# Optimization experiments

Measured on AMD Instinct MI355X. Metric: run time of the kernel, lower is better.

The kernel has to match this reference:

```python
import jax, jax.numpy as jnp
import numpy as np

N, DIM, TOPK = 8192, 512, 10


def setup_inputs() -> dict:
    key = jax.random.key(0)
    k1, k2, k3, k4, k5 = jax.random.split(key, 5)
    s = DIM ** -0.5
    return {
        "X": jax.random.normal(k1, (N, DIM), dtype=jnp.float32),
        "Wh": jax.random.normal(k2, (DIM, DIM), dtype=jnp.float32) * s,
        "bh": jax.random.normal(k3, (DIM,), dtype=jnp.float32) * s,
        "Wt": jax.random.normal(k4, (DIM, DIM), dtype=jnp.float32) * s,
        "bt": jax.random.normal(k5, (DIM,), dtype=jnp.float32) * s,
    }


def reference(X, Wh, bh, Wt, bt):
    n, dim = X.shape
    scale = dim ** -0.5
    e_h = X @ Wh.T + bh                      # [n, dim]
    e_t = X @ Wt.T + bt                      # [n, dim]
    logits = (e_h @ e_t.T) * scale           # [n, n]
    topk_val, topk_idx = jax.lax.top_k(logits, TOPK)   # [n, k]
    weights = jax.nn.softmax(topk_val, axis=-1)        # [n, k]
    src = jnp.repeat(jnp.arange(n, dtype=jnp.int32), TOPK)  # [n*k]
    dst = topk_idx.reshape(-1).astype(jnp.int32)
    edge_index = jnp.stack([src, dst], axis=0)          # [2, n*k]
    edge_weight = weights.reshape(-1)                   # [n*k]
    return edge_index, edge_weight
```

## Files before the change

kernel.cpp:

```cpp
#include <hip/hip_runtime.h>
#include <math.h>

#define NROWS 8192
#define DIMK  512
#define TOPK  10
#define SCALE 0.044194173824159223f

#define ETM 128
#define ETN 128
#define ETK 16
#define NTHREADS 256

#define BM 128
#define BN 256
#define BK 32
#define NS2 16
#define SCOLS2 (NROWS / NS2)
#define NQ 256
#define CAP 64
#define TMARGIN 2.0f

typedef __attribute__((ext_vector_type(8))) short bf16x8;
typedef __attribute__((ext_vector_type(4))) float f32x4;
typedef __attribute__((ext_vector_type(2))) float f32x2;

__device__ __forceinline__ unsigned short f2bf(float f) {
  unsigned int u = __float_as_uint(f);
  u = (u + 0x7FFF + ((u >> 16) & 1)) >> 16;
  return (unsigned short)u;
}

__device__ __forceinline__ void gld16(const void* g, const void* lds) {
  __builtin_amdgcn_global_load_lds(
      (const __attribute__((address_space(1))) void*)g,
      (__attribute__((address_space(3))) void*)lds, 16, 0, 0);
}

__device__ __forceinline__ f32x2 pk_fma(f32x2 a, f32x2 b, f32x2 c) {
#if __has_builtin(__builtin_elementwise_fma)
  return __builtin_elementwise_fma(a, b, c);
#else
  f32x2 r; r[0] = fmaf(a[0], b[0], c[0]); r[1] = fmaf(a[1], b[1], c[1]);
  return r;
#endif
}

__global__ __launch_bounds__(NTHREADS, 2)
void embed_gemm(const float* __restrict__ X,
                const float* __restrict__ Wh, const float* __restrict__ bh,
                const float* __restrict__ Wt, const float* __restrict__ bt,
                float* __restrict__ Eh, float* __restrict__ Et,
                unsigned short* __restrict__ Ehb, unsigned short* __restrict__ Etb) {
  __shared__ float As[2][ETK][ETM + 4];
  __shared__ float Bs[2][ETK][ETN + 4];

  const int tid = threadIdx.x;
  const int rowBase = blockIdx.x * ETM;
  const int colBase = blockIdx.y * ETN;
  const float* W  = (colBase < DIMK) ? Wh : Wt;
  const float* bb = (colBase < DIMK) ? bh : bt;
  float* Out            = (colBase < DIMK) ? Eh : Et;
  unsigned short* Outb  = (colBase < DIMK) ? Ehb : Etb;
  const int colOff = colBase & (DIMK - 1);

  const int tx = tid & 15, ty = tid >> 4;
  f32x2 acc2[8][4];
#pragma unroll
  for (int r = 0; r < 8; ++r)
#pragma unroll
    for (int p = 0; p < 4; ++p) acc2[r][p] = (f32x2){0.f, 0.f};

  auto stage = [&](int buf, int kt) {
#pragma unroll
    for (int u = 0; u < 2; ++u) {
      const int idx = tid + u * NTHREADS;
      const int r = idx >> 2;
      const int dc = idx & 3;
      const float4 av = *(const float4*)&X[(size_t)(rowBase + r) * DIMK + kt + dc * 4];
      As[buf][dc * 4 + 0][r] = av.x; As[buf][dc * 4 + 1][r] = av.y;
      As[buf][dc * 4 + 2][r] = av.z; As[buf][dc * 4 + 3][r] = av.w;
    }
#pragma unroll
    for (int u = 0; u < 2; ++u) {
      const int idx = tid + u * NTHREADS;
      const int r = idx >> 2;
      const int dc = idx & 3;
      const float4 bv = *(const float4*)&W[(size_t)(colOff + r) * DIMK + kt + dc * 4];
      Bs[buf][dc * 4 + 0][r] = bv.x; Bs[buf][dc * 4 + 1][r] = bv.y;
      Bs[buf][dc * 4 + 2][r] = bv.z; Bs[buf][dc * 4 + 3][r] = bv.w;
    }
  };
  auto compute = [&](int buf) {
#pragma unroll 4
    for (int k = 0; k < ETK; ++k) {
      const float4 a0 = *(const float4*)&As[buf][k][ty * 4];
      const float4 a1 = *(const float4*)&As[buf][k][64 + ty * 4];
      const float4 b0 = *(const float4*)&Bs[buf][k][tx * 4];
      const float4 b1 = *(const float4*)&Bs[buf][k][64 + tx * 4];
      const float ar[8] = {a0.x, a0.y, a0.z, a0.w, a1.x, a1.y, a1.z, a1.w};
      const f32x2 bp[4] = {(f32x2){b0.x, b0.y}, (f32x2){b0.z, b0.w},
                           (f32x2){b1.x, b1.y}, (f32x2){b1.z, b1.w}};
#pragma unroll
      for (int r = 0; r < 8; ++r) {
        const f32x2 ar2 = (f32x2){ar[r], ar[r]};
#pragma unroll
        for (int p = 0; p < 4; ++p)
          acc2[r][p] = pk_fma(ar2, bp[p], acc2[r][p]);
      }
    }
  };

  stage(0, 0);
  __syncthreads();
#pragma unroll 1
  for (int ki = 0; ki < DIMK / ETK; ki += 2) {
    if (ki + 1 < DIMK / ETK) stage(1, (ki + 1) * ETK);
    compute(0);
    __syncthreads();
    if (ki + 2 < DIMK / ETK) stage(0, (ki + 2) * ETK);
    compute(1);
    __syncthreads();
  }

  float br[8];
  {
    const float4 bv0 = *(const float4*)&bb[colOff + tx * 4];
    const float4 bv1 = *(const float4*)&bb[colOff + 64 + tx * 4];
    br[0] = bv0.x; br[1] = bv0.y; br[2] = bv0.z; br[3] = bv0.w;
    br[4] = bv1.x; br[5] = bv1.y; br[6] = bv1.z; br[7] = bv1.w;
  }
#pragma unroll
  for (int r = 0; r < 8; ++r) {
    const int row = rowBase + ((r < 4) ? (ty * 4 + r) : (64 + ty * 4 + r - 4));
    float4 o0, o1;
    o0.x = acc2[r][0][0] + br[0]; o0.y = acc2[r][0][1] + br[1];
    o0.z = acc2[r][1][0] + br[2]; o0.w = acc2[r][1][1] + br[3];
    o1.x = acc2[r][2][0] + br[4]; o1.y = acc2[r][2][1] + br[5];
    o1.z = acc2[r][3][0] + br[6]; o1.w = acc2[r][3][1] + br[7];
    const size_t off0 = (size_t)row * DIMK + colOff + tx * 4;
    const size_t off1 = off0 + 64;
    *(float4*)&Out[off0] = o0;
    *(float4*)&Out[off1] = o1;
    ushort4 q0, q1;
    q0.x = f2bf(o0.x); q0.y = f2bf(o0.y); q0.z = f2bf(o0.z); q0.w = f2bf(o0.w);
    q1.x = f2bf(o1.x); q1.y = f2bf(o1.y); q1.z = f2bf(o1.z); q1.w = f2bf(o1.w);
    *(ushort4*)&Outb[off0] = q0;
    *(ushort4*)&Outb[off1] = q1;
  }
}

__global__ __launch_bounds__(256, 2)
void screen_store(const unsigned short* __restrict__ Ehb,
                  const unsigned short* __restrict__ Etb,
                  float* __restrict__ tmax, unsigned short* __restrict__ Sc) {
  __shared__ unsigned short pool[2 * BM * BK + 2 * BN * BK];
  unsigned short* const AsP[2] = {pool, pool + BM * BK};
  unsigned short* const BsP[2] = {pool + 2 * BM * BK, pool + 2 * BM * BK + BN * BK};
  unsigned short* const Csb = pool;

  const int tid = threadIdx.x;
  const int rowBase = blockIdx.x * BM;
  const int strip = blockIdx.y;
  const int w = tid >> 6, lane = tid & 63;
  const int q = lane >> 4, l15 = lane & 15;
  const int wr = (w & 1) * 64, wc = (w >> 1) * 128;
  const int rr = tid >> 1, hq = tid & 1;

  const int wb0 = __builtin_amdgcn_readfirstlane(tid & ~63);
  const int ar0 = tid >> 2,         ac0 = (tid & 3) * 8;
  const int ar1 = (tid + 256) >> 2, ac1 = ((tid + 256) & 3) * 8;

  for (int ct = 0; ct < SCOLS2; ct += BN) {
    const int colBase = strip * SCOLS2 + ct;
    f32x4 acc[4][8];
#pragma unroll
    for (int i = 0; i < 4; ++i)
#pragma unroll
      for (int j = 0; j < 8; ++j) acc[i][j] = (f32x4){0.f, 0.f, 0.f, 0.f};

    auto stage = [&](int buf, int kt) {
      gld16(Ehb + (size_t)(rowBase + ar0) * DIMK + kt + ac0, AsP[buf] + wb0 * 8);
      gld16(Ehb + (size_t)(rowBase + ar1) * DIMK + kt + ac1, AsP[buf] + (wb0 + 256) * 8);
#pragma unroll
      for (int u = 0; u < 4; ++u) {
        const int c = tid + u * 256;
        gld16(Etb + (size_t)(colBase + (c >> 2)) * DIMK + kt + (c & 3) * 8,
              BsP[buf] + (wb0 + u * 256) * 8);
      }
    };
    auto compute = [&](int buf) {
      bf16x8 af[4], bf[8];
#pragma unroll
      for (int i = 0; i < 4; ++i)
        af[i] = *(const bf16x8*)&AsP[buf][(wr + i * 16 + l15) * BK + q * 8];
#pragma unroll
      for (int j = 0; j < 8; ++j)
        bf[j] = *(const bf16x8*)&BsP[buf][(wc + j * 16 + l15) * BK + q * 8];
#pragma unroll
      for (int i = 0; i < 4; ++i)
#pragma unroll
        for (int j = 0; j < 8; ++j)
          acc[i][j] = __builtin_amdgcn_mfma_f32_16x16x32_bf16(af[i], bf[j], acc[i][j], 0, 0, 0);
    };

    stage(0, 0);
    __syncthreads();
#pragma unroll 1
    for (int ki = 0; ki < DIMK / BK; ki += 2) {
      if (ki + 1 < DIMK / BK) stage(1, (ki + 1) * BK);
      compute(0);
      __syncthreads();
      if (ki + 2 < DIMK / BK) stage(0, (ki + 2) * BK);
      compute(1);
      __syncthreads();
    }

#pragma unroll
    for (int qtr = 0; qtr < 4; ++qtr) {
      const int jbase = (qtr & 1) * 4;
      if ((w >> 1) == (qtr >> 1)) {
#pragma unroll
        for (int i = 0; i < 4; ++i)
#pragma unroll
          for (int jj = 0; jj < 4; ++jj)
#pragma unroll
            for (int rg = 0; rg < 4; ++rg)
              Csb[(wr + i * 16 + q * 4 + rg) * 72 + jj * 16 + l15] =
                  f2bf(acc[i][jbase + jj][rg]);
      }
      __syncthreads();
      float m = -INFINITY;
      uint4 buf4[4];
#pragma unroll
      for (int k = 0; k < 4; ++k) {
        buf4[k] = *(const uint4*)&Csb[rr * 72 + hq * 32 + k * 8];
        const unsigned int uu[4] = {buf4[k].x, buf4[k].y, buf4[k].z, buf4[k].w};
#pragma unroll
        for (int e = 0; e < 4; ++e) {
          m = fmaxf(m, __uint_as_float(uu[e] << 16));
          m = fmaxf(m, __uint_as_float(uu[e] & 0xFFFF0000u));
        }
      }
      const int gbase = (colBase + qtr * 64) >> 5;
      tmax[(size_t)(rowBase + rr) * NQ + gbase + hq] = m;
      uint4* dst = (uint4*)&Sc[(size_t)(rowBase + rr) * NROWS + colBase + qtr * 64 + hq * 32];
#pragma unroll
      for (int k = 0; k < 4; ++k) dst[k] = buf4[k];
      __syncthreads();
    }
  }
}

__global__ __launch_bounds__(256)
void collect_rescore(const unsigned short* __restrict__ Sc,
                     const float* __restrict__ tmax,
                     const float* __restrict__ Eh, const float* __restrict__ Et,
                     float* __restrict__ out) {
  __shared__ float tm[NQ];
  __shared__ float tts;
  __shared__ int lcnt;
  __shared__ int lcand[CAP];
  const int tid = threadIdx.x;
  const int lane = tid & 63;
  const int wid = tid >> 6;
  const int r = blockIdx.x;

  if (tid == 0) lcnt = 0;
  tm[tid] = tmax[(size_t)r * NQ + tid];
  __syncthreads();

  if (wid == 0) {
    float a0 = tm[lane * 4 + 0], a1 = tm[lane * 4 + 1];
    float a2 = tm[lane * 4 + 2], a3 = tm[lane * 4 + 3];
    float g = -INFINITY;
#pragma unroll 1
    for (int j = 0; j < TOPK; ++j) {
      const float lm = fmaxf(fmaxf(a0, a1), fmaxf(a2, a3));
      g = lm;
#pragma unroll
      for (int off = 32; off > 0; off >>= 1) g = fmaxf(g, __shfl_xor(g, off, 64));
      const unsigned long long ball = __ballot(lm == g);
      const int src = __ffsll((long long)ball) - 1;
      if (lane == src) {
        if      (a0 == g) a0 = -INFINITY;
        else if (a1 == g) a1 = -INFINITY;
        else if (a2 == g) a2 = -INFINITY;
        else              a3 = -INFINITY;
      }
    }
    if (lane == 0) tts = g - TMARGIN;
  }
  __syncthreads();
  const float tt = tts;

  if (tm[tid] >= tt) {
    const unsigned short* chunk = Sc + (size_t)r * NROWS + tid * 32;
#pragma unroll
    for (int k = 0; k < 4; ++k) {
      const uint4 u = *(const uint4*)&chunk[k * 8];
      const unsigned int uu[4] = {u.x, u.y, u.z, u.w};
#pragma unroll
      for (int e = 0; e < 4; ++e) {
        const float lo = __uint_as_float(uu[e] << 16);
        const float hi = __uint_as_float(uu[e] & 0xFFFF0000u);
        const int c0 = tid * 32 + k * 8 + 2 * e;
        if (lo >= tt) {
          const int p = atomicAdd(&lcnt, 1);
          if (p < CAP) lcand[p] = c0;
        }
        if (hi >= tt) {
          const int p = atomicAdd(&lcnt, 1);
          if (p < CAP) lcand[p] = c0 + 1;
        }
      }
    }
  }
  __syncthreads();
  if (wid != 0) return;

  const int n = min(lcnt, CAP);
  const bool active = lane < n;
  const int col = active ? lcand[lane] : 0;

  const float* a = Eh + (size_t)r * DIMK;
  const float* b = Et + (size_t)col * DIMK;
  float p = 0.f;
#pragma unroll 4
  for (int k = 0; k < DIMK; k += 4) {
    const float4 av = *(const float4*)&a[k];
    const float4 bv = *(const float4*)&b[k];
    p = fmaf(av.x, bv.x, p);
    p = fmaf(av.y, bv.y, p);
    p = fmaf(av.z, bv.z, p);
    p = fmaf(av.w, bv.w, p);
  }
  float v = active ? p * SCALE : -INFINITY;
  const int vc = active ? col : 0x7FFFFFFF;

  float myv = -INFINITY; int myc = 0; float m = 0.f;
  float vv = v; int cc2 = vc;
#pragma unroll 1
  for (int j = 0; j < TOPK; ++j) {
    float bvv = vv; int bcc = cc2;
#pragma unroll
    for (int off = 32; off > 0; off >>= 1) {
      const float ov = __shfl_xor(bvv, off, 64);
      const int oc = __shfl_xor(bcc, off, 64);
      if (ov > bvv || (ov == bvv && oc < bcc)) { bvv = ov; bcc = oc; }
    }
    if (j == 0) m = bvv;
    if (lane == j) { myv = bvv; myc = bcc; }
    if (vv == bvv && cc2 == bcc) vv = -INFINITY;
  }

  float sum = 0.f;
#pragma unroll
  for (int j = 0; j < TOPK; ++j) sum += expf(__shfl(myv, j, 64) - m);
  const float inv = 1.0f / sum;

  if (lane < TOPK) {
    const size_t ro = (size_t)r * TOPK + lane;
    out[ro] = (float)r;
    out[(size_t)NROWS * TOPK + ro] = (float)myc;
    out[2 * (size_t)NROWS * TOPK + ro] = expf(myv - m) * inv;
  }
}

extern "C" void kernel_launch(void* const* d_in, const int* in_sizes, int n_in,
                              void* d_out, int out_size, void* d_ws, size_t ws_size,
                              hipStream_t stream) {
  const float* X  = (const float*)d_in[0];
  const float* Wh = (const float*)d_in[1];
  const float* bh = (const float*)d_in[2];
  const float* Wt = (const float*)d_in[3];
  const float* bt = (const float*)d_in[4];
  float* out = (float*)d_out;

  char* ws = (char*)d_ws;
  const size_t embB  = (size_t)NROWS * DIMK * sizeof(float);
  const size_t embBH = (size_t)NROWS * DIMK * sizeof(unsigned short);
  const size_t tmaxB = (size_t)NROWS * NQ * sizeof(float);
  float* Eh   = (float*)ws;
  float* Et   = (float*)(ws + embB);
  unsigned short* Ehb = (unsigned short*)(ws + 2 * embB);
  unsigned short* Etb = (unsigned short*)(ws + 2 * embB + embBH);
  float* tmax = (float*)(ws + 2 * embB + 2 * embBH);
  unsigned short* Sc = (unsigned short*)(ws + 2 * embB + 2 * embBH + tmaxB);

  dim3 blk(NTHREADS);
  dim3 g1(NROWS / ETM, (2 * DIMK) / ETN);
  embed_gemm<<<g1, blk, 0, stream>>>(X, Wh, bh, Wt, bt, Eh, Et, Ehb, Etb);

  dim3 g2(NROWS / BM, NS2);
  screen_store<<<g2, blk, 0, stream>>>(Ehb, Etb, tmax, Sc);

  collect_rescore<<<NROWS, blk, 0, stream>>>(Sc, tmax, Eh, Et, out);
}
```

Before: 361.3 us.

## Process one row per wavefront in collect_rescore instead of one row per block

The collect/rescore kernel now assigns each of the four wavefronts in a block its own row, with per-wave candidate lists and counters. Previously three of the four waves only helped with the candidate scan and then sat idle during the top-k threshold search and the rescoring. The change drops the block-wide barriers and launches a quarter as many blocks, so every wave does rescoring work. In exchange, each wave scans its qualifying chunks serially, and LDS atomics on the shared counter within a wave may contend.

```diff
diff --git a/kernel.cpp b/kernel.cpp
--- a/kernel.cpp
+++ b/kernel.cpp
@@ -256,71 +256,65 @@
                      const float* __restrict__ tmax,
                      const float* __restrict__ Eh, const float* __restrict__ Et,
                      float* __restrict__ out) {
-  __shared__ float tm[NQ];
-  __shared__ float tts;
-  __shared__ int lcnt;
-  __shared__ int lcand[CAP];
-  const int tid = threadIdx.x;
-  const int lane = tid & 63;
-  const int wid = tid >> 6;
-  const int r = blockIdx.x;
-
-  if (tid == 0) lcnt = 0;
-  tm[tid] = tmax[(size_t)r * NQ + tid];
-  __syncthreads();
-
-  if (wid == 0) {
-    float a0 = tm[lane * 4 + 0], a1 = tm[lane * 4 + 1];
-    float a2 = tm[lane * 4 + 2], a3 = tm[lane * 4 + 3];
-    float g = -INFINITY;
+  __shared__ int lcnt[4];
+  __shared__ int lcand[4][CAP];
+  const int lane = threadIdx.x & 63;
+  const int wid = threadIdx.x >> 6;
+  const int r = blockIdx.x * 4 + wid;
+
+  if (lane == 0) lcnt[wid] = 0;
+
+  const f32x4 gm = *(const f32x4*)&tmax[(size_t)r * NQ + lane * 4];
+
+  float a0 = gm[0], a1 = gm[1], a2 = gm[2], a3 = gm[3];
+  float g = -INFINITY;
 #pragma unroll 1
-    for (int j = 0; j < TOPK; ++j) {
-      const float lm = fmaxf(fmaxf(a0, a1), fmaxf(a2, a3));
-      g = lm;
-#pragma unroll
-      for (int off = 32; off > 0; off >>= 1) g = fmaxf(g, __shfl_xor(g, off, 64));
-      const unsigned long long ball = __ballot(lm == g);
-      const int src = __ffsll((long long)ball) - 1;
-      if (lane == src) {
-        if      (a0 == g) a0 = -INFINITY;
-        else if (a1 == g) a1 = -INFINITY;
-        else if (a2 == g) a2 = -INFINITY;
-        else              a3 = -INFINITY;
-      }
-    }
-    if (lane == 0) tts = g - TMARGIN;
-  }
-  __syncthreads();
-  const float tt = tts;
-
-  if (tm[tid] >= tt) {
-    const unsigned short* chunk = Sc + (size_t)r * NROWS + tid * 32;
-#pragma unroll
-    for (int k = 0; k < 4; ++k) {
-      const uint4 u = *(const uint4*)&chunk[k * 8];
-      const unsigned int uu[4] = {u.x, u.y, u.z, u.w};
-#pragma unroll
-      for (int e = 0; e < 4; ++e) {
-        const float lo = __uint_as_float(uu[e] << 16);
-        const float hi = __uint_as_float(uu[e] & 0xFFFF0000u);
-        const int c0 = tid * 32 + k * 8 + 2 * e;
-        if (lo >= tt) {
-          const int p = atomicAdd(&lcnt, 1);
-          if (p < CAP) lcand[p] = c0;
+  for (int j = 0; j < TOPK; ++j) {
+    const float lm = fmaxf(fmaxf(a0, a1), fmaxf(a2, a3));
+    g = lm;
+#pragma unroll
+    for (int off = 32; off > 0; off >>= 1) g = fmaxf(g, __shfl_xor(g, off, 64));
+    const unsigned long long ball = __ballot(lm == g);
+    const int src = __ffsll((long long)ball) - 1;
+    if (lane == src) {
+      if      (a0 == g) a0 = -INFINITY;
+      else if (a1 == g) a1 = -INFINITY;
+      else if (a2 == g) a2 = -INFINITY;
+      else              a3 = -INFINITY;
+    }
+  }
+  const float tt = g - TMARGIN;
+
+  const unsigned short* row = Sc + (size_t)r * NROWS;
+#pragma unroll
+  for (int e = 0; e < 4; ++e) {
+    if (gm[e] >= tt) {
+      const int cbase = (lane * 4 + e) * 32;
+#pragma unroll
+      for (int k = 0; k < 4; ++k) {
+        const uint4 u = *(const uint4*)&row[cbase + k * 8];
+        const unsigned int uu[4] = {u.x, u.y, u.z, u.w};
+#pragma unroll
+        for (int x = 0; x < 4; ++x) {
+          const float lo = __uint_as_float(uu[x] << 16);
+          const float hi = __uint_as_float(uu[x] & 0xFFFF0000u);
+          const int c0 = cbase + k * 8 + 2 * x;
+          if (lo >= tt) {
+            const int p = atomicAdd(&lcnt[wid], 1);
+            if (p < CAP) lcand[wid][p] = c0;
+          }
+          if (hi >= tt) {
+            const int p = atomicAdd(&lcnt[wid], 1);
+            if (p < CAP) lcand[wid][p] = c0 + 1;
+          }
         }
-        if (hi >= tt) {
-          const int p = atomicAdd(&lcnt, 1);
-          if (p < CAP) lcand[p] = c0 + 1;
-        }
-      }
-    }
-  }
-  __syncthreads();
-  if (wid != 0) return;
-
-  const int n = min(lcnt, CAP);
+      }
+    }
+  }
+
+  const int n = min(lcnt[wid], CAP);
   const bool active = lane < n;
-  const int col = active ? lcand[lane] : 0;
+  const int col = active ? lcand[wid][lane] : 0;
 
   const float* a = Eh + (size_t)r * DIMK;
   const float* b = Et + (size_t)col * DIMK;
@@ -394,5 +388,5 @@
   dim3 g2(NROWS / BM, NS2);
   screen_store<<<g2, blk, 0, stream>>>(Ehb, Etb, tmax, Sc);
 
-  collect_rescore<<<NROWS, blk, 0, stream>>>(Sc, tmax, Eh, Et, out);
-}
+  collect_rescore<<<NROWS / 4, blk, 0, stream>>>(Sc, tmax, Eh, Et, out);
+}
```

Result: slower. 372.4 us (+3.1%).
